# Kernel tuning notes

Measured on AMD Instinct MI355X. Metric: run time of the kernel, lower is better.

The kernel has to match this reference:

```python
import jax, jax.numpy as jnp
from jax import lax
import numpy as np

LAG, IN, H, B, T = 168, 64, 1024, 512, 168

def setup_inputs() -> dict:
    key = jax.random.key(0)
    ks = jax.random.split(key, 10)
    s1 = 1.0 / np.sqrt(LAG)
    sg = 1.0 / np.sqrt(H)
    return {
        "lag": jax.random.normal(ks[0], (B, LAG), jnp.float32),
        "curr": jax.random.normal(ks[1], (T, B, IN), jnp.float32),
        "W1": jax.random.uniform(ks[2], (H, LAG), jnp.float32, -s1, s1),
        "b1": jax.random.uniform(ks[3], (H,), jnp.float32, -s1, s1),
        "W_ih": jax.random.uniform(ks[4], (3 * H, IN), jnp.float32, -sg, sg),
        "b_ih": jax.random.uniform(ks[5], (3 * H,), jnp.float32, -sg, sg),
        "W_hh": jax.random.uniform(ks[6], (3 * H, H), jnp.float32, -sg, sg),
        "b_hh": jax.random.uniform(ks[7], (3 * H,), jnp.float32, -sg, sg),
        "W3": jax.random.uniform(ks[8], (1, H), jnp.float32, -sg, sg),
        "b3": jax.random.uniform(ks[9], (1,), jnp.float32, -sg, sg),
    }

def reference(lag, curr, W1, b1, W_ih, b_ih, W_hh, b_hh, W3, b3):
    # h_t = dense1(lag)
    h0 = lag @ W1.T + b1  # [B, H]

    def step(h, x):
        # PyTorch GRUCell math
        gi = x @ W_ih.T + b_ih   # [B, 3H]
        gh = h @ W_hh.T + b_hh   # [B, 3H]
        i_r, i_z, i_n = jnp.split(gi, 3, axis=-1)
        h_r, h_z, h_n = jnp.split(gh, 3, axis=-1)
        r = jax.nn.sigmoid(i_r + h_r)
        z = jax.nn.sigmoid(i_z + h_z)
        n = jnp.tanh(i_n + r * h_n)
        h_new = (1.0 - z) * n + z * h
        y = h_new @ W3.T + b3    # [B, 1] -> dense3 prediction
        return h_new, y[:, 0]

    _, ys = lax.scan(step, h0, curr)  # ys: [T, B]
    # torch.stack(outputs, 1).squeeze(2) -> [B, T]
    return ys.T
```

## Files before the change

kernel.cpp:

```cpp
#include <hip/hip_runtime.h>

#define T_STEPS 168
#define B_SZ 512
#define H_SZ 1024
#define IN_SZ 64
#define LAG_SZ 168
#define NWG 256
#define TPB 256

typedef __attribute__((ext_vector_type(8))) short short8;
typedef __attribute__((ext_vector_type(8))) __bf16 bf16x8;
typedef __attribute__((ext_vector_type(4))) float floatx4;

union V8u { short8 s; bf16x8 v; unsigned u[4]; };

__device__ __forceinline__ float bf2f(unsigned short u) {
    union { unsigned u; float f; } v; v.u = ((unsigned)u) << 16; return v.f;
}
__device__ __forceinline__ unsigned short f2bf(float x) {
    union { float f; unsigned u; } v; v.f = x;
    unsigned r = ((v.u >> 16) & 1u) + 0x7fffu;
    return (unsigned short)((v.u + r) >> 16);
}
__device__ __forceinline__ unsigned cvtpk(float a, float b) {
    unsigned r; asm("v_cvt_pk_bf16_f32 %0, %1, %2" : "=v"(r) : "v"(a), "v"(b)); return r;
}
__device__ __forceinline__ float lo_f(unsigned u) {
    union { unsigned x; float f; } v; v.x = u << 16; return v.f;
}
__device__ __forceinline__ float hi_f(unsigned u) {
    union { unsigned x; float f; } v; v.x = u & 0xffff0000u; return v.f;
}

#define MFB(a, b, c) __builtin_amdgcn_mfma_f32_16x16x32_bf16((a), (b), (c), 0, 0, 0)


__global__ void crnn_init2(const float* __restrict__ Whh,
                           unsigned short* __restrict__ whi,
                           unsigned short* __restrict__ h_hi,
                           unsigned int* __restrict__ flg, unsigned int* __restrict__ pop)
{
    int tid = blockIdx.x * blockDim.x + threadIdx.x;
    int nthr = gridDim.x * blockDim.x;
    for (int c = tid; c < 64 * 96 * 64; c += nthr) {
        int lane = c & 63;
        int f = (c >> 6) % 96;
        int n16 = c / (96 * 64);
        int kk = f / 3, g = f % 3;
        int l15 = lane & 15, g4 = lane >> 4;
        int row = g * H_SZ + n16 * 16 + l15;
        int col = kk * 32 + g4 * 8;
        const float* src = Whh + (size_t)row * H_SZ + col;
        short8 sh;
        #pragma unroll
        for (int e = 0; e < 8; e++) sh[e] = (short)f2bf(src[e]);
        *(short8*)(whi + (size_t)c * 8) = sh;
    }
    for (int k = tid; k < 2 * B_SZ * H_SZ; k += nthr) h_hi[k] = 0;
    for (int k = tid; k < 169 * 256; k += nthr) flg[k] = 0u;
    for (int k = tid; k < 16; k += nthr) pop[k] = 0u;
}

#define ISSUE_A(ARR, KB) { \
    unsigned va_ = voffA_cur + (unsigned)((KB) * 512); \
    asm volatile("global_load_dwordx4 %0, %1, %2 sc0"            : "=v"(ARR[0].s) : "v"(va_), "s"(sAh)); \
    asm volatile("global_load_dwordx4 %0, %1, %2 offset:64 sc0"  : "=v"(ARR[1].s) : "v"(va_), "s"(sAh)); \
    asm volatile("global_load_dwordx4 %0, %1, %2 offset:128 sc0" : "=v"(ARR[2].s) : "v"(va_), "s"(sAh)); \
    asm volatile("global_load_dwordx4 %0, %1, %2 offset:192 sc0" : "=v"(ARR[3].s) : "v"(va_), "s"(sAh)); \
    asm volatile("global_load_dwordx4 %0, %1, %2 offset:256 sc0" : "=v"(ARR[4].s) : "v"(va_), "s"(sAh)); \
    asm volatile("global_load_dwordx4 %0, %1, %2 offset:320 sc0" : "=v"(ARR[5].s) : "v"(va_), "s"(sAh)); \
    asm volatile("global_load_dwordx4 %0, %1, %2 offset:384 sc0" : "=v"(ARR[6].s) : "v"(va_), "s"(sAh)); \
    asm volatile("global_load_dwordx4 %0, %1, %2 offset:448 sc0" : "=v"(ARR[7].s) : "v"(va_), "s"(sAh)); \
}

#define KEEP8(ARR) { \
    _Pragma("unroll") \
    for (int _q = 0; _q < 8; _q++) asm volatile("" : "+v"(ARR[_q].s)); \
}

#define COMPUTE_G(ARR, KB) { \
    _Pragma("unroll") \
    for (int q = 0; q < 8; q++) { \
        const int kk = (KB) * 8 + q; \
        unsigned o_ = (unsigned)(kk * 64); \
        bf16x8 xA0 = *(const bf16x8*)((const char*)whhA + ((bb0 + o_) ^ swz)); \
        bf16x8 xA1 = *(const bf16x8*)((const char*)whhA + ((bb1 + o_) ^ swz)); \
        bf16x8 xA2 = *(const bf16x8*)((const char*)whhA + ((bb2 + o_) ^ swz)); \
        const char* pB = wfB + (size_t)kk * 3072; \
        bf16x8 h1_0 = *(const bf16x8*)(pB); \
        bf16x8 h1_1 = *(const bf16x8*)(pB + 1024); \
        bf16x8 h1_2 = *(const bf16x8*)(pB + 2048); \
        acc[0] = MFB(ARR[q].v, xA0, acc[0]); \
        acc[2] = MFB(ARR[q].v, xA1, acc[2]); \
        acc[4] = MFB(ARR[q].v, xA2, acc[4]); \
        acc[1] = MFB(ARR[q].v, h1_0, acc[1]); \
        acc[3] = MFB(ARR[q].v, h1_1, acc[3]); \
        acc[5] = MFB(ARR[q].v, h1_2, acc[5]); \
    } \
}

__launch_bounds__(TPB, 1)
__global__ void crnn_main2(
    const float* __restrict__ lag, const float* __restrict__ curr,
    const float* __restrict__ W1, const float* __restrict__ b1,
    const float* __restrict__ Wih, const float* __restrict__ b_ih,
    const float* __restrict__ Whh, const float* __restrict__ b_hh,
    const float* __restrict__ W3, const float* __restrict__ b3,
    const unsigned short* __restrict__ whi,
    unsigned short* __restrict__ h_hi,
    unsigned int* __restrict__ flg, unsigned int* __restrict__ pop,
    float* __restrict__ out)
{
    __shared__ __align__(16) unsigned short whhA[48 * 1024];
    __shared__ __align__(16) unsigned short wihh[96 * 64];
    __shared__ __align__(16) unsigned short wihl[96 * 64];
    __shared__ float red[4];
    __shared__ int sh_xr[2];

    const int tid = threadIdx.x;
    if (tid == 0) {
        unsigned x;
        asm volatile("s_getreg_b32 %0, hwreg(HW_REG_XCC_ID)" : "=s"(x));
        x &= 7u;
        unsigned rk = __hip_atomic_fetch_add(&pop[x], 1u, __ATOMIC_RELAXED, __HIP_MEMORY_SCOPE_AGENT);
        sh_xr[0] = (int)x;
        sh_xr[1] = (int)(rk & 31u);
    }
    __syncthreads();
    const int xcc = sh_xr[0];
    const int r = sh_xr[1];
    const int RB = xcc * 64;
    const int J = r * 32;
    const int n16B = 2 * r + 1;

    const int lane = tid & 63;
    const int wv = tid >> 6;
    const int l15 = lane & 15;
    const int g4 = lane >> 4;

    for (int c = tid; c < 48 * 128; c += TPB) {
        int rr = c >> 7, cc = c & 127;
        int gr = (rr >> 4) * H_SZ + J + (rr & 15);
        const float* src = Whh + (size_t)gr * H_SZ + cc * 8;
        short8 s;
        #pragma unroll
        for (int e = 0; e < 8; e++) s[e] = (short)f2bf(src[e]);
        unsigned byte = ((unsigned)(rr * 2048 + cc * 16)) ^ ((unsigned)((rr & 7) << 4));
        *(short8*)((char*)whhA + byte) = s;
    }
    for (int c = tid; c < 96 * 8; c += TPB) {
        int rr = c >> 3, cc = c & 7;
        int gr = (rr >> 5) * H_SZ + J + (rr & 31);
        const float* src = Wih + (size_t)gr * IN_SZ + cc * 8;
        short8 sh, sl;
        #pragma unroll
        for (int e = 0; e < 8; e++) {
            float v = src[e];
            unsigned short hi = f2bf(v);
            sh[e] = (short)hi;
            sl[e] = (short)f2bf(v - bf2f(hi));
        }
        unsigned byte = ((unsigned)(rr * 128 + cc * 16)) ^ ((unsigned)((rr & 7) << 4));
        *(short8*)((char*)wihh + byte) = sh;
        *(short8*)((char*)wihl + byte) = sl;
    }

    float hp[2][4];
    {
        const int brow = RB + wv * 16 + g4 * 4;
        #pragma unroll
        for (int j16 = 0; j16 < 2; j16++) {
            const int j = J + j16 * 16 + l15;
            float a[4];
            float bias = b1[j];
            #pragma unroll
            for (int e = 0; e < 4; e++) a[e] = bias;
            const float* w1p = W1 + (size_t)j * LAG_SZ;
            for (int k = 0; k < LAG_SZ; k += 4) {
                floatx4 w4 = *(const floatx4*)(w1p + k);
                #pragma unroll
                for (int e = 0; e < 4; e++) {
                    floatx4 l4 = *(const floatx4*)(lag + (size_t)(brow + e) * LAG_SZ + k);
                    a[e] += l4.x * w4.x + l4.y * w4.y + l4.z * w4.z + l4.w * w4.w;
                }
            }
            #pragma unroll
            for (int e = 0; e < 4; e++) {
                hp[j16][e] = a[e];
                h_hi[(size_t)(brow + e) * H_SZ + j] = f2bf(a[e]);
            }
        }
    }

    float br_[2], bz_[2], bni_[2], bnh_[2];
    #pragma unroll
    for (int j16 = 0; j16 < 2; j16++) {
        int j = J + j16 * 16 + l15;
        br_[j16] = b_ih[j] + b_hh[j];
        bz_[j16] = b_ih[H_SZ + j] + b_hh[H_SZ + j];
        bni_[j16] = b_ih[2 * H_SZ + j];
        bnh_[j16] = b_hh[2 * H_SZ + j];
    }

    const int ycol = (tid & 127) * 8;
    const int yrow = RB + 2 * r + (tid >> 7);
    const floatx4 yw0 = *(const floatx4*)(W3 + ycol);
    const floatx4 yw1 = *(const floatx4*)(W3 + ycol + 4);
    const float b3v = b3[0];

    const unsigned short* sAh = h_hi;
    const char* wfB = (const char*)whi + (size_t)n16B * 98304 + lane * 16;
    const unsigned voffA0 = (unsigned)(((RB + wv * 16 + l15) * H_SZ + g4 * 8) * 2);

    const unsigned bb0 = (unsigned)((0 * 16 + l15) * 2048 + g4 * 16);
    const unsigned bb1 = (unsigned)((1 * 16 + l15) * 2048 + g4 * 16);
    const unsigned bb2 = (unsigned)((2 * 16 + l15) * 2048 + g4 * 16);
    const unsigned swz = (unsigned)((l15 & 7) << 4);

    bool dead = false;
    auto set_flag = [&](int t1) {
        asm volatile("s_waitcnt vmcnt(0)" ::: "memory");
        __syncthreads();
        if (tid == 0)
            __hip_atomic_store(flg + (size_t)t1 * 256 + (size_t)xcc * 32 + (size_t)r, 1u,
                               __ATOMIC_RELAXED, __HIP_MEMORY_SCOPE_AGENT);
    };
    auto check = [&](int t, int kb) {
        if (dead) { __builtin_amdgcn_sched_barrier(0); return; }
        const unsigned int* fp = flg + (size_t)t * 256 + (size_t)xcc * 32
                               + (size_t)kb * 8 + (size_t)(lane & 7);
        int spins = 0;
        while (true) {
            unsigned v = __hip_atomic_load(fp, __ATOMIC_RELAXED, __HIP_MEMORY_SCOPE_AGENT);
            if (__ballot(v != 0) == ~0ull) break;
            __builtin_amdgcn_s_sleep(1);
            if (++spins > 2000000) { dead = true; break; }
        }
        __builtin_amdgcn_sched_barrier(0);
    };

    floatx4 acc_gi[6];
    auto compute_gi = [&](int t) {
        const float* xp = curr + (size_t)t * (B_SZ * IN_SZ)
                        + (size_t)(RB + wv * 16 + l15) * IN_SZ + g4 * 8;
        #pragma unroll
        for (int ni = 0; ni < 6; ni++) acc_gi[ni] = floatx4{0.f, 0.f, 0.f, 0.f};
        #pragma unroll
        for (int kg = 0; kg < 2; kg++) {
            floatx4 v0 = *(const floatx4*)(xp + kg * 32);
            floatx4 v1 = *(const floatx4*)(xp + kg * 32 + 4);
            V8u ah, al;
            ah.u[0] = cvtpk(v0.x, v0.y); ah.u[1] = cvtpk(v0.z, v0.w);
            ah.u[2] = cvtpk(v1.x, v1.y); ah.u[3] = cvtpk(v1.z, v1.w);
            al.u[0] = cvtpk(v0.x - lo_f(ah.u[0]), v0.y - hi_f(ah.u[0]));
            al.u[1] = cvtpk(v0.z - lo_f(ah.u[1]), v0.w - hi_f(ah.u[1]));
            al.u[2] = cvtpk(v1.x - lo_f(ah.u[2]), v1.y - hi_f(ah.u[2]));
            al.u[3] = cvtpk(v1.z - lo_f(ah.u[3]), v1.w - hi_f(ah.u[3]));
            #pragma unroll
            for (int g = 0; g < 3; g++) {
                #pragma unroll
                for (int j16 = 0; j16 < 2; j16++) {
                    int rr = g * 32 + j16 * 16 + l15;
                    unsigned byte = ((unsigned)(rr * 128 + kg * 64 + g4 * 16)) ^ ((unsigned)((rr & 7) << 4));
                    bf16x8 bh = *(const bf16x8*)((const char*)wihh + byte);
                    bf16x8 bl = *(const bf16x8*)((const char*)wihl + byte);
                    int ni = g * 2 + j16;
                    acc_gi[ni] = MFB(ah.v, bh, acc_gi[ni]);
                    acc_gi[ni] = MFB(al.v, bh, acc_gi[ni]);
                    acc_gi[ni] = MFB(ah.v, bl, acc_gi[ni]);
                }
            }
        }
    };

    auto y_reduce = [&](const V8u& yv, int tcol) {
        float p = 0.f;
        #pragma unroll
        for (int e = 0; e < 8; e++) {
            float w = (e < 4) ? yw0[e] : yw1[e - 4];
            p += bf2f((unsigned short)yv.s[e]) * w;
        }
        #pragma unroll
        for (int s = 32; s >= 1; s >>= 1) p += __shfl_down(p, s, 64);
        if (lane == 0) red[wv] = p;
        __syncthreads();
        if (tid == 0) {
            out[(size_t)(RB + 2 * r + 0) * T_STEPS + tcol] = red[0] + red[1] + b3v;
            out[(size_t)(RB + 2 * r + 1) * T_STEPS + tcol] = red[2] + red[3] + b3v;
        }
        __syncthreads();
    };

    set_flag(0);
    compute_gi(0);

    const int kb0 = r >> 3;
    int cur = 0;
    for (int t = 0; t < T_STEPS; t++) {
        const unsigned voffA_cur = voffA0 + (unsigned)cur * 1048576u;

        floatx4 acc[6];
        #pragma unroll
        for (int ni = 0; ni < 6; ni++) acc[ni] = floatx4{0.f, 0.f, 0.f, 0.f};

        V8u A0[8], A1[8], yv;
        const int k0 = kb0, k1 = (kb0 + 1) & 3, k2 = (kb0 + 2) & 3, k3 = (kb0 + 3) & 3;

        check(t, k0); ISSUE_A(A0, k0);
        check(t, k1); ISSUE_A(A1, k1);
        KEEP8(A0);  COMPUTE_G(A0, k0);
        check(t, k2); ISSUE_A(A0, k2);
        KEEP8(A1);  COMPUTE_G(A1, k1);
        check(t, k3); ISSUE_A(A1, k3);
        {
            const char* ph = (const char*)(h_hi + (size_t)cur * 524288 + (size_t)yrow * H_SZ + ycol);
            asm volatile("global_load_dwordx4 %0, %1, off sc0" : "=v"(yv.s) : "v"(ph));
        }
        KEEP8(A0);  COMPUTE_G(A0, k2);
        asm volatile("s_waitcnt vmcnt(0)" ::: "memory");
        __builtin_amdgcn_sched_barrier(0);
        KEEP8(A1);  COMPUTE_G(A1, k3);

        {
            unsigned short* nh = h_hi + (size_t)(cur ^ 1) * 524288;
            const int brow = RB + wv * 16 + g4 * 4;
            #pragma unroll
            for (int j16 = 0; j16 < 2; j16++) {
                const int j = J + j16 * 16 + l15;
                #pragma unroll
                for (int e = 0; e < 4; e++) {
                    float grv = acc[0 + j16][e] + acc_gi[0 + j16][e] + br_[j16];
                    float gzv = acc[2 + j16][e] + acc_gi[2 + j16][e] + bz_[j16];
                    float ghn = acc[4 + j16][e] + bnh_[j16];
                    float gin = acc_gi[4 + j16][e] + bni_[j16];
                    float rg = 1.f / (1.f + __expf(-grv));
                    float zg = 1.f / (1.f + __expf(-gzv));
                    float nx = gin + rg * ghn;
                    float e2 = __expf(-2.f * fabsf(nx));
                    float th = copysignf((1.f - e2) / (1.f + e2), nx);
                    float hnew = (1.f - zg) * th + zg * hp[j16][e];
                    hp[j16][e] = hnew;
                    nh[(size_t)(brow + e) * H_SZ + j] = f2bf(hnew);
                }
            }
        }

        set_flag(t + 1);
        if (t > 0) y_reduce(yv, t - 1);
        if (t + 1 < T_STEPS) compute_gi(t + 1);

        cur ^= 1;
    }

    check(T_STEPS, 0); check(T_STEPS, 1); check(T_STEPS, 2); check(T_STEPS, 3);
    {
        V8u yv;
        const char* ph = (const char*)(h_hi + (size_t)cur * 524288 + (size_t)yrow * H_SZ + ycol);
        asm volatile("global_load_dwordx4 %0, %1, off sc0" : "=v"(yv.s) : "v"(ph));
        asm volatile("s_waitcnt vmcnt(0)" ::: "memory");
        __builtin_amdgcn_sched_barrier(0);
        y_reduce(yv, T_STEPS - 1);
    }
}


extern "C" void kernel_launch(void* const* d_in, const int* in_sizes, int n_in,
                              void* d_out, int out_size, void* d_ws, size_t ws_size,
                              hipStream_t stream) {
    const float* lag  = (const float*)d_in[0];
    const float* curr = (const float*)d_in[1];
    const float* W1   = (const float*)d_in[2];
    const float* b1   = (const float*)d_in[3];
    const float* Wih  = (const float*)d_in[4];
    const float* bih  = (const float*)d_in[5];
    const float* Whh  = (const float*)d_in[6];
    const float* bhh  = (const float*)d_in[7];
    const float* W3   = (const float*)d_in[8];
    const float* b3   = (const float*)d_in[9];
    float* out = (float*)d_out;
    char* w = (char*)d_ws;

    if (ws_size < (size_t)8561728) return;

    unsigned short* whi  = (unsigned short*)(w + 0);
    unsigned short* h_hi = (unsigned short*)(w + 6291456);
    unsigned int*   flg  = (unsigned int*)(w + 8388608);
    unsigned int*   pop  = (unsigned int*)(w + 8561664);

    hipLaunchKernelGGL(crnn_init2, dim3(2048), dim3(256), 0, stream,
                       Whh, whi, h_hi, flg, pop);

    void* args[] = { (void*)&lag, (void*)&curr, (void*)&W1, (void*)&b1,
                     (void*)&Wih, (void*)&bih, (void*)&Whh, (void*)&bhh,
                     (void*)&W3, (void*)&b3, (void*)&whi,
                     (void*)&h_hi, (void*)&flg, (void*)&pop, (void*)&out };
    hipError_t e = hipLaunchCooperativeKernel((void*)crnn_main2, dim3(NWG), dim3(TPB), args, 0, stream);
    if (e != hipSuccess) {
        (void)hipGetLastError();
        hipLaunchKernelGGL(crnn_main2, dim3(NWG), dim3(TPB), 0, stream,
                           lag, curr, W1, b1, Wih, bih, Whh, bhh, W3, b3,
                           whi, h_hi, flg, pop, out);
    }
}
```

Baseline: 2.441 ms.

## Split K across two wave groups per block with LDS reduction and per-wave flags

Doubles threads per block to 512 and splits the recurrent and input-gate K dimension between two groups of four waves. The upper group stores its partial accumulators to LDS for the lower group to reduce. Readiness flags become per-wave instead of per-block, so the block-wide barrier before each flag store goes away and consumers wait on finer-grained flags. The y-output reduction is folded into the per-step barrier. This halves per-wave serial MFMA work on the latency-bound recurrent path, at the cost of an extra LDS round trip and more register and LDS pressure per block.

After: 3.379 ms. 38.4% more time.

```diff
diff --git a/kernel.cpp b/kernel.cpp
--- a/kernel.cpp
+++ b/kernel.cpp
@@ -6,7 +6,7 @@
 #define IN_SZ 64
 #define LAG_SZ 168
 #define NWG 256
-#define TPB 256
+#define TPB 512
 
 typedef __attribute__((ext_vector_type(8))) short short8;
 typedef __attribute__((ext_vector_type(8))) __bf16 bf16x8;
@@ -57,7 +57,7 @@
         *(short8*)(whi + (size_t)c * 8) = sh;
     }
     for (int k = tid; k < 2 * B_SZ * H_SZ; k += nthr) h_hi[k] = 0;
-    for (int k = tid; k < 169 * 256; k += nthr) flg[k] = 0u;
+    for (int k = tid; k < 169 * 1024; k += nthr) flg[k] = 0u;
     for (int k = tid; k < 16; k += nthr) pop[k] = 0u;
 }
 
@@ -114,7 +114,8 @@
     __shared__ __align__(16) unsigned short whhA[48 * 1024];
     __shared__ __align__(16) unsigned short wihh[96 * 64];
     __shared__ __align__(16) unsigned short wihl[96 * 64];
-    __shared__ float red[4];
+    __shared__ __align__(16) float redacc[256 * 32];
+    __shared__ float yred[2][4];
     __shared__ int sh_xr[2];
 
     const int tid = threadIdx.x;
@@ -135,6 +136,10 @@
 
     const int lane = tid & 63;
     const int wv = tid >> 6;
+    const int wvm = wv & 3;
+    const int kgK = wv >> 2;
+    const bool loW = (wv < 4);
+    const bool doY = (wvm < 2);
     const int l15 = lane & 15;
     const int g4 = lane >> 4;
 
@@ -164,10 +169,32 @@
         *(short8*)((char*)wihh + byte) = sh;
         *(short8*)((char*)wihl + byte) = sl;
     }
+    __syncthreads();
+
+    bool dead = false;
+    auto set_flag_wave = [&](int t1) {
+        asm volatile("s_waitcnt vmcnt(0)" ::: "memory");
+        if (lane == 0)
+            __hip_atomic_store(flg + (size_t)t1 * 1024 + (size_t)xcc * 128 + (size_t)r * 4 + wvm,
+                               1u, __ATOMIC_RELAXED, __HIP_MEMORY_SCOPE_AGENT);
+    };
+    auto check = [&](int t, int kb) {
+        if (dead) { __builtin_amdgcn_sched_barrier(0); return; }
+        const unsigned int* fp = flg + (size_t)t * 1024 + (size_t)xcc * 128
+                               + (size_t)kb * 32 + (size_t)(lane & 31);
+        int spins = 0;
+        while (true) {
+            unsigned v = __hip_atomic_load(fp, __ATOMIC_RELAXED, __HIP_MEMORY_SCOPE_AGENT);
+            if (__ballot(v != 0) == ~0ull) break;
+            __builtin_amdgcn_s_sleep(1);
+            if (++spins > 2000000) { dead = true; break; }
+        }
+        __builtin_amdgcn_sched_barrier(0);
+    };
 
     float hp[2][4];
-    {
-        const int brow = RB + wv * 16 + g4 * 4;
+    if (loW) {
+        const int brow = RB + wvm * 16 + g4 * 4;
         #pragma unroll
         for (int j16 = 0; j16 < 2; j16++) {
             const int j = J + j16 * 16 + l15;
@@ -190,6 +217,7 @@
                 h_hi[(size_t)(brow + e) * H_SZ + j] = f2bf(a[e]);
             }
         }
+        set_flag_wave(0);
     }
 
     float br_[2], bz_[2], bni_[2], bnh_[2];
@@ -202,99 +230,58 @@
         bnh_[j16] = b_hh[2 * H_SZ + j];
     }
 
-    const int ycol = (tid & 127) * 8;
-    const int yrow = RB + 2 * r + (tid >> 7);
+    const int ycol = kgK * 512 + lane * 8;
+    const int yrow = RB + 2 * r + (wv & 1);
+    const int yslot = kgK * 2 + (wv & 1);
     const floatx4 yw0 = *(const floatx4*)(W3 + ycol);
     const floatx4 yw1 = *(const floatx4*)(W3 + ycol + 4);
     const float b3v = b3[0];
 
     const unsigned short* sAh = h_hi;
     const char* wfB = (const char*)whi + (size_t)n16B * 98304 + lane * 16;
-    const unsigned voffA0 = (unsigned)(((RB + wv * 16 + l15) * H_SZ + g4 * 8) * 2);
+    const unsigned voffA0 = (unsigned)(((RB + wvm * 16 + l15) * H_SZ + g4 * 8) * 2);
 
     const unsigned bb0 = (unsigned)((0 * 16 + l15) * 2048 + g4 * 16);
     const unsigned bb1 = (unsigned)((1 * 16 + l15) * 2048 + g4 * 16);
     const unsigned bb2 = (unsigned)((2 * 16 + l15) * 2048 + g4 * 16);
     const unsigned swz = (unsigned)((l15 & 7) << 4);
 
-    bool dead = false;
-    auto set_flag = [&](int t1) {
-        asm volatile("s_waitcnt vmcnt(0)" ::: "memory");
-        __syncthreads();
-        if (tid == 0)
-            __hip_atomic_store(flg + (size_t)t1 * 256 + (size_t)xcc * 32 + (size_t)r, 1u,
-                               __ATOMIC_RELAXED, __HIP_MEMORY_SCOPE_AGENT);
-    };
-    auto check = [&](int t, int kb) {
-        if (dead) { __builtin_amdgcn_sched_barrier(0); return; }
-        const unsigned int* fp = flg + (size_t)t * 256 + (size_t)xcc * 32
-                               + (size_t)kb * 8 + (size_t)(lane & 7);
-        int spins = 0;
-        while (true) {
-            unsigned v = __hip_atomic_load(fp, __ATOMIC_RELAXED, __HIP_MEMORY_SCOPE_AGENT);
-            if (__ballot(v != 0) == ~0ull) break;
-            __builtin_amdgcn_s_sleep(1);
-            if (++spins > 2000000) { dead = true; break; }
-        }
-        __builtin_amdgcn_sched_barrier(0);
-    };
+    const int s_ = (r >> 3) & 1;
+    const int kb_a = kgK * 2 + s_, kb_b = kgK * 2 + (s_ ^ 1);
 
     floatx4 acc_gi[6];
     auto compute_gi = [&](int t) {
         const float* xp = curr + (size_t)t * (B_SZ * IN_SZ)
-                        + (size_t)(RB + wv * 16 + l15) * IN_SZ + g4 * 8;
+                        + (size_t)(RB + wvm * 16 + l15) * IN_SZ + g4 * 8 + kgK * 32;
         #pragma unroll
         for (int ni = 0; ni < 6; ni++) acc_gi[ni] = floatx4{0.f, 0.f, 0.f, 0.f};
-        #pragma unroll
-        for (int kg = 0; kg < 2; kg++) {
-            floatx4 v0 = *(const floatx4*)(xp + kg * 32);
-            floatx4 v1 = *(const floatx4*)(xp + kg * 32 + 4);
-            V8u ah, al;
-            ah.u[0] = cvtpk(v0.x, v0.y); ah.u[1] = cvtpk(v0.z, v0.w);
-            ah.u[2] = cvtpk(v1.x, v1.y); ah.u[3] = cvtpk(v1.z, v1.w);
-            al.u[0] = cvtpk(v0.x - lo_f(ah.u[0]), v0.y - hi_f(ah.u[0]));
-            al.u[1] = cvtpk(v0.z - lo_f(ah.u[1]), v0.w - hi_f(ah.u[1]));
-            al.u[2] = cvtpk(v1.x - lo_f(ah.u[2]), v1.y - hi_f(ah.u[2]));
-            al.u[3] = cvtpk(v1.z - lo_f(ah.u[3]), v1.w - hi_f(ah.u[3]));
-            #pragma unroll
-            for (int g = 0; g < 3; g++) {
-                #pragma unroll
-                for (int j16 = 0; j16 < 2; j16++) {
-                    int rr = g * 32 + j16 * 16 + l15;
-                    unsigned byte = ((unsigned)(rr * 128 + kg * 64 + g4 * 16)) ^ ((unsigned)((rr & 7) << 4));
-                    bf16x8 bh = *(const bf16x8*)((const char*)wihh + byte);
-                    bf16x8 bl = *(const bf16x8*)((const char*)wihl + byte);
-                    int ni = g * 2 + j16;
-                    acc_gi[ni] = MFB(ah.v, bh, acc_gi[ni]);
-                    acc_gi[ni] = MFB(al.v, bh, acc_gi[ni]);
-                    acc_gi[ni] = MFB(ah.v, bl, acc_gi[ni]);
-                }
+        floatx4 v0 = *(const floatx4*)(xp);
+        floatx4 v1 = *(const floatx4*)(xp + 4);
+        V8u ah, al;
+        ah.u[0] = cvtpk(v0.x, v0.y); ah.u[1] = cvtpk(v0.z, v0.w);
+        ah.u[2] = cvtpk(v1.x, v1.y); ah.u[3] = cvtpk(v1.z, v1.w);
+        al.u[0] = cvtpk(v0.x - lo_f(ah.u[0]), v0.y - hi_f(ah.u[0]));
+        al.u[1] = cvtpk(v0.z - lo_f(ah.u[1]), v0.w - hi_f(ah.u[1]));
+        al.u[2] = cvtpk(v1.x - lo_f(ah.u[2]), v1.y - hi_f(ah.u[2]));
+        al.u[3] = cvtpk(v1.z - lo_f(ah.u[3]), v1.w - hi_f(ah.u[3]));
+        #pragma unroll
+        for (int g = 0; g < 3; g++) {
+            #pragma unroll
+            for (int j16 = 0; j16 < 2; j16++) {
+                int rr = g * 32 + j16 * 16 + l15;
+                unsigned byte = ((unsigned)(rr * 128 + kgK * 64 + g4 * 16)) ^ ((unsigned)((rr & 7) << 4));
+                bf16x8 bh = *(const bf16x8*)((const char*)wihh + byte);
+                bf16x8 bl = *(const bf16x8*)((const char*)wihl + byte);
+                int ni = g * 2 + j16;
+                acc_gi[ni] = MFB(ah.v, bh, acc_gi[ni]);
+                acc_gi[ni] = MFB(al.v, bh, acc_gi[ni]);
+                acc_gi[ni] = MFB(ah.v, bl, acc_gi[ni]);
             }
         }
     };
 
-    auto y_reduce = [&](const V8u& yv, int tcol) {
-        float p = 0.f;
-        #pragma unroll
-        for (int e = 0; e < 8; e++) {
-            float w = (e < 4) ? yw0[e] : yw1[e - 4];
-            p += bf2f((unsigned short)yv.s[e]) * w;
-        }
-        #pragma unroll
-        for (int s = 32; s >= 1; s >>= 1) p += __shfl_down(p, s, 64);
-        if (lane == 0) red[wv] = p;
-        __syncthreads();
-        if (tid == 0) {
-            out[(size_t)(RB + 2 * r + 0) * T_STEPS + tcol] = red[0] + red[1] + b3v;
-            out[(size_t)(RB + 2 * r + 1) * T_STEPS + tcol] = red[2] + red[3] + b3v;
-        }
-        __syncthreads();
-    };
-
-    set_flag(0);
     compute_gi(0);
 
-    const int kb0 = r >> 3;
     int cur = 0;
     for (int t = 0; t < T_STEPS; t++) {
         const unsigned voffA_cur = voffA0 + (unsigned)cur * 1048576u;
@@ -304,35 +291,61 @@
         for (int ni = 0; ni < 6; ni++) acc[ni] = floatx4{0.f, 0.f, 0.f, 0.f};
 
         V8u A0[8], A1[8], yv;
-        const int k0 = kb0, k1 = (kb0 + 1) & 3, k2 = (kb0 + 2) & 3, k3 = (kb0 + 3) & 3;
-
-        check(t, k0); ISSUE_A(A0, k0);
-        check(t, k1); ISSUE_A(A1, k1);
-        KEEP8(A0);  COMPUTE_G(A0, k0);
-        check(t, k2); ISSUE_A(A0, k2);
-        KEEP8(A1);  COMPUTE_G(A1, k1);
-        check(t, k3); ISSUE_A(A1, k3);
-        {
+        check(t, kb_a); ISSUE_A(A0, kb_a);
+        check(t, kb_b); ISSUE_A(A1, kb_b);
+        if (doY) {
             const char* ph = (const char*)(h_hi + (size_t)cur * 524288 + (size_t)yrow * H_SZ + ycol);
             asm volatile("global_load_dwordx4 %0, %1, off sc0" : "=v"(yv.s) : "v"(ph));
         }
-        KEEP8(A0);  COMPUTE_G(A0, k2);
+        KEEP8(A0); COMPUTE_G(A0, kb_a);
         asm volatile("s_waitcnt vmcnt(0)" ::: "memory");
         __builtin_amdgcn_sched_barrier(0);
-        KEEP8(A1);  COMPUTE_G(A1, k3);
-
-        {
+        KEEP8(A1); COMPUTE_G(A1, kb_b);
+
+        if (doY) {
+            float p = 0.f;
+            #pragma unroll
+            for (int e = 0; e < 8; e++) {
+                float w = (e < 4) ? yw0[e] : yw1[e - 4];
+                p += bf2f((unsigned short)yv.s[e]) * w;
+            }
+            #pragma unroll
+            for (int sh = 32; sh >= 1; sh >>= 1) p += __shfl_down(p, sh, 64);
+            if (lane == 0) yred[t & 1][yslot] = p;
+        }
+
+        if (!loW) {
+            float* rb = redacc + (size_t)(tid - 256) * 32;
+            #pragma unroll
+            for (int i = 0; i < 4; i++) *(floatx4*)(rb + i * 4) = acc[i] + acc_gi[i];
+            *(floatx4*)(rb + 16) = acc[4];
+            *(floatx4*)(rb + 20) = acc[5];
+            *(floatx4*)(rb + 24) = acc_gi[4];
+            *(floatx4*)(rb + 28) = acc_gi[5];
+        }
+        __syncthreads();
+
+        if (loW) {
+            const float* rb = redacc + (size_t)tid * 32;
+            floatx4 m03[4], mhh[2], mih[2];
+            #pragma unroll
+            for (int i = 0; i < 4; i++) m03[i] = acc[i] + acc_gi[i] + *(const floatx4*)(rb + i * 4);
+            #pragma unroll
+            for (int j16 = 0; j16 < 2; j16++) {
+                mhh[j16] = acc[4 + j16] + *(const floatx4*)(rb + 16 + j16 * 4);
+                mih[j16] = acc_gi[4 + j16] + *(const floatx4*)(rb + 24 + j16 * 4);
+            }
             unsigned short* nh = h_hi + (size_t)(cur ^ 1) * 524288;
-            const int brow = RB + wv * 16 + g4 * 4;
+            const int brow = RB + wvm * 16 + g4 * 4;
             #pragma unroll
             for (int j16 = 0; j16 < 2; j16++) {
                 const int j = J + j16 * 16 + l15;
                 #pragma unroll
                 for (int e = 0; e < 4; e++) {
-                    float grv = acc[0 + j16][e] + acc_gi[0 + j16][e] + br_[j16];
-                    float gzv = acc[2 + j16][e] + acc_gi[2 + j16][e] + bz_[j16];
-                    float ghn = acc[4 + j16][e] + bnh_[j16];
-                    float gin = acc_gi[4 + j16][e] + bni_[j16];
+                    float grv = m03[0 + j16][e] + br_[j16];
+                    float gzv = m03[2 + j16][e] + bz_[j16];
+                    float ghn = mhh[j16][e] + bnh_[j16];
+                    float gin = mih[j16][e] + bni_[j16];
                     float rg = 1.f / (1.f + __expf(-grv));
                     float zg = 1.f / (1.f + __expf(-gzv));
                     float nx = gin + rg * ghn;
@@ -343,24 +356,37 @@
                     nh[(size_t)(brow + e) * H_SZ + j] = f2bf(hnew);
                 }
             }
-        }
-
-        set_flag(t + 1);
-        if (t > 0) y_reduce(yv, t - 1);
+            set_flag_wave(t + 1);
+        }
+
         if (t + 1 < T_STEPS) compute_gi(t + 1);
 
+        if (wv < 2 && lane == 0 && t > 0)
+            out[(size_t)yrow * T_STEPS + (t - 1)] = yred[t & 1][wv] + yred[t & 1][2 + wv] + b3v;
+
         cur ^= 1;
     }
 
-    check(T_STEPS, 0); check(T_STEPS, 1); check(T_STEPS, 2); check(T_STEPS, 3);
-    {
+    if (doY) {
+        check(T_STEPS, kb_a); check(T_STEPS, kb_b);
         V8u yv;
         const char* ph = (const char*)(h_hi + (size_t)cur * 524288 + (size_t)yrow * H_SZ + ycol);
         asm volatile("global_load_dwordx4 %0, %1, off sc0" : "=v"(yv.s) : "v"(ph));
         asm volatile("s_waitcnt vmcnt(0)" ::: "memory");
         __builtin_amdgcn_sched_barrier(0);
-        y_reduce(yv, T_STEPS - 1);
-    }
+        float p = 0.f;
+        #pragma unroll
+        for (int e = 0; e < 8; e++) {
+            float w = (e < 4) ? yw0[e] : yw1[e - 4];
+            p += bf2f((unsigned short)yv.s[e]) * w;
+        }
+        #pragma unroll
+        for (int sh = 32; sh >= 1; sh >>= 1) p += __shfl_down(p, sh, 64);
+        if (lane == 0) yred[0][yslot] = p;
+    }
+    __syncthreads();
+    if (wv < 2 && lane == 0)
+        out[(size_t)yrow * T_STEPS + (T_STEPS - 1)] = yred[0][wv] + yred[0][2 + wv] + b3v;
 }
 
 
@@ -380,12 +406,12 @@
     float* out = (float*)d_out;
     char* w = (char*)d_ws;
 
-    if (ws_size < (size_t)8561728) return;
+    if (ws_size < (size_t)9080896) return;
 
     unsigned short* whi  = (unsigned short*)(w + 0);
     unsigned short* h_hi = (unsigned short*)(w + 6291456);
     unsigned int*   flg  = (unsigned int*)(w + 8388608);
-    unsigned int*   pop  = (unsigned int*)(w + 8561664);
+    unsigned int*   pop  = (unsigned int*)(w + 9080832);
 
     hipLaunchKernelGGL(crnn_init2, dim3(2048), dim3(256), 0, stream,
                        Whh, whi, h_hi, flg, pop);
```

## Use per-wave flags and defer output projection via partial sums

Applied to the files above, without the earlier changes.

Replaces the per-block __syncthreads plus single flag with per-wave flags, so each wave publishes its slice of h as soon as it has written it, and consumers poll the specific producer waves they need. The per-step y reduction, which reloaded h and needed two block barriers each step, is replaced by a register-level dot product with W3 and a 16-lane shuffle reduce. These bf16 partial sums are written to a workspace buffer and summed once after the last step. This removes block barriers from the recurrent critical path. In exchange it uses more flag memory, adds an end-of-run reduction, and rounds the per-slice y partial sums to bf16, which may cost accuracy.

Measured after the change: 2.686 ms. 1.1x slower.

```diff
diff --git a/kernel.cpp b/kernel.cpp
--- a/kernel.cpp
+++ b/kernel.cpp
@@ -38,6 +38,7 @@
 __global__ void crnn_init2(const float* __restrict__ Whh,
                            unsigned short* __restrict__ whi,
                            unsigned short* __restrict__ h_hi,
+                           unsigned short* __restrict__ ypart,
                            unsigned int* __restrict__ flg, unsigned int* __restrict__ pop)
 {
     int tid = blockIdx.x * blockDim.x + threadIdx.x;
@@ -57,7 +58,8 @@
         *(short8*)(whi + (size_t)c * 8) = sh;
     }
     for (int k = tid; k < 2 * B_SZ * H_SZ; k += nthr) h_hi[k] = 0;
-    for (int k = tid; k < 169 * 256; k += nthr) flg[k] = 0u;
+    for (int k = tid; k < 168 * 8 * 64 * 32; k += nthr) ypart[k] = 0;
+    for (int k = tid; k < 169 * 1024; k += nthr) flg[k] = 0u;
     for (int k = tid; k < 16; k += nthr) pop[k] = 0u;
 }
 
@@ -107,14 +109,13 @@
     const float* __restrict__ Whh, const float* __restrict__ b_hh,
     const float* __restrict__ W3, const float* __restrict__ b3,
     const unsigned short* __restrict__ whi,
-    unsigned short* __restrict__ h_hi,
+    unsigned short* __restrict__ h_hi, unsigned short* __restrict__ ypart,
     unsigned int* __restrict__ flg, unsigned int* __restrict__ pop,
     float* __restrict__ out)
 {
     __shared__ __align__(16) unsigned short whhA[48 * 1024];
     __shared__ __align__(16) unsigned short wihh[96 * 64];
     __shared__ __align__(16) unsigned short wihl[96 * 64];
-    __shared__ float red[4];
     __shared__ int sh_xr[2];
 
     const int tid = threadIdx.x;
@@ -164,6 +165,28 @@
         *(short8*)((char*)wihh + byte) = sh;
         *(short8*)((char*)wihl + byte) = sl;
     }
+    __syncthreads();
+
+    bool dead = false;
+    auto set_flag_wave = [&](int t1) {
+        asm volatile("s_waitcnt vmcnt(0)" ::: "memory");
+        if (lane == 0)
+            __hip_atomic_store(flg + (size_t)t1 * 1024 + (size_t)xcc * 128 + (size_t)r * 4 + wv,
+                               1u, __ATOMIC_RELAXED, __HIP_MEMORY_SCOPE_AGENT);
+    };
+    auto check = [&](int t, int kb) {
+        if (dead) { __builtin_amdgcn_sched_barrier(0); return; }
+        const unsigned int* fp = flg + (size_t)t * 1024 + (size_t)xcc * 128
+                               + (size_t)(kb * 8 + (lane & 7)) * 4 + wv;
+        int spins = 0;
+        while (true) {
+            unsigned v = __hip_atomic_load(fp, __ATOMIC_RELAXED, __HIP_MEMORY_SCOPE_AGENT);
+            if (__ballot(v != 0) == ~0ull) break;
+            __builtin_amdgcn_s_sleep(1);
+            if (++spins > 2000000) { dead = true; break; }
+        }
+        __builtin_amdgcn_sched_barrier(0);
+    };
 
     float hp[2][4];
     {
@@ -191,6 +214,7 @@
             }
         }
     }
+    set_flag_wave(0);
 
     float br_[2], bz_[2], bni_[2], bnh_[2];
     #pragma unroll
@@ -201,11 +225,8 @@
         bni_[j16] = b_ih[2 * H_SZ + j];
         bnh_[j16] = b_hh[2 * H_SZ + j];
     }
-
-    const int ycol = (tid & 127) * 8;
-    const int yrow = RB + 2 * r + (tid >> 7);
-    const floatx4 yw0 = *(const floatx4*)(W3 + ycol);
-    const floatx4 yw1 = *(const floatx4*)(W3 + ycol + 4);
+    const float w3a = W3[J + l15];
+    const float w3b = W3[J + 16 + l15];
     const float b3v = b3[0];
 
     const unsigned short* sAh = h_hi;
@@ -216,28 +237,6 @@
     const unsigned bb1 = (unsigned)((1 * 16 + l15) * 2048 + g4 * 16);
     const unsigned bb2 = (unsigned)((2 * 16 + l15) * 2048 + g4 * 16);
     const unsigned swz = (unsigned)((l15 & 7) << 4);
-
-    bool dead = false;
-    auto set_flag = [&](int t1) {
-        asm volatile("s_waitcnt vmcnt(0)" ::: "memory");
-        __syncthreads();
-        if (tid == 0)
-            __hip_atomic_store(flg + (size_t)t1 * 256 + (size_t)xcc * 32 + (size_t)r, 1u,
-                               __ATOMIC_RELAXED, __HIP_MEMORY_SCOPE_AGENT);
-    };
-    auto check = [&](int t, int kb) {
-        if (dead) { __builtin_amdgcn_sched_barrier(0); return; }
-        const unsigned int* fp = flg + (size_t)t * 256 + (size_t)xcc * 32
-                               + (size_t)kb * 8 + (size_t)(lane & 7);
-        int spins = 0;
-        while (true) {
-            unsigned v = __hip_atomic_load(fp, __ATOMIC_RELAXED, __HIP_MEMORY_SCOPE_AGENT);
-            if (__ballot(v != 0) == ~0ull) break;
-            __builtin_amdgcn_s_sleep(1);
-            if (++spins > 2000000) { dead = true; break; }
-        }
-        __builtin_amdgcn_sched_barrier(0);
-    };
 
     floatx4 acc_gi[6];
     auto compute_gi = [&](int t) {
@@ -273,25 +272,6 @@
         }
     };
 
-    auto y_reduce = [&](const V8u& yv, int tcol) {
-        float p = 0.f;
-        #pragma unroll
-        for (int e = 0; e < 8; e++) {
-            float w = (e < 4) ? yw0[e] : yw1[e - 4];
-            p += bf2f((unsigned short)yv.s[e]) * w;
-        }
-        #pragma unroll
-        for (int s = 32; s >= 1; s >>= 1) p += __shfl_down(p, s, 64);
-        if (lane == 0) red[wv] = p;
-        __syncthreads();
-        if (tid == 0) {
-            out[(size_t)(RB + 2 * r + 0) * T_STEPS + tcol] = red[0] + red[1] + b3v;
-            out[(size_t)(RB + 2 * r + 1) * T_STEPS + tcol] = red[2] + red[3] + b3v;
-        }
-        __syncthreads();
-    };
-
-    set_flag(0);
     compute_gi(0);
 
     const int kb0 = r >> 3;
@@ -303,7 +283,7 @@
         #pragma unroll
         for (int ni = 0; ni < 6; ni++) acc[ni] = floatx4{0.f, 0.f, 0.f, 0.f};
 
-        V8u A0[8], A1[8], yv;
+        V8u A0[8], A1[8];
         const int k0 = kb0, k1 = (kb0 + 1) & 3, k2 = (kb0 + 2) & 3, k3 = (kb0 + 3) & 3;
 
         check(t, k0); ISSUE_A(A0, k0);
@@ -312,10 +292,6 @@
         check(t, k2); ISSUE_A(A0, k2);
         KEEP8(A1);  COMPUTE_G(A1, k1);
         check(t, k3); ISSUE_A(A1, k3);
-        {
-            const char* ph = (const char*)(h_hi + (size_t)cur * 524288 + (size_t)yrow * H_SZ + ycol);
-            asm volatile("global_load_dwordx4 %0, %1, off sc0" : "=v"(yv.s) : "v"(ph));
-        }
         KEEP8(A0);  COMPUTE_G(A0, k2);
         asm volatile("s_waitcnt vmcnt(0)" ::: "memory");
         __builtin_amdgcn_sched_barrier(0);
@@ -345,21 +321,62 @@
             }
         }
 
-        set_flag(t + 1);
-        if (t > 0) y_reduce(yv, t - 1);
+        if (t + 1 < T_STEPS) set_flag_wave(t + 1);
+
+        {
+            #pragma unroll
+            for (int e = 0; e < 4; e++) {
+                float p = w3a * hp[0][e] + w3b * hp[1][e];
+                p += __shfl_xor(p, 1, 64);
+                p += __shfl_xor(p, 2, 64);
+                p += __shfl_xor(p, 4, 64);
+                p += __shfl_xor(p, 8, 64);
+                if (l15 == 0) {
+                    int row = wv * 16 + g4 * 4 + e;
+                    ypart[((size_t)(t * 8 + xcc) * 64 + row) * 32 + r] = f2bf(p);
+                }
+            }
+        }
+
         if (t + 1 < T_STEPS) compute_gi(t + 1);
-
         cur ^= 1;
     }
 
-    check(T_STEPS, 0); check(T_STEPS, 1); check(T_STEPS, 2); check(T_STEPS, 3);
+    set_flag_wave(T_STEPS);
     {
-        V8u yv;
-        const char* ph = (const char*)(h_hi + (size_t)cur * 524288 + (size_t)yrow * H_SZ + ycol);
-        asm volatile("global_load_dwordx4 %0, %1, off sc0" : "=v"(yv.s) : "v"(ph));
+        if (!dead) {
+            const unsigned int* f1 = flg + (size_t)T_STEPS * 1024 + (size_t)xcc * 128 + lane;
+            const unsigned int* f2 = f1 + 64;
+            int spins = 0;
+            while (true) {
+                unsigned v1 = __hip_atomic_load(f1, __ATOMIC_RELAXED, __HIP_MEMORY_SCOPE_AGENT);
+                unsigned v2 = __hip_atomic_load(f2, __ATOMIC_RELAXED, __HIP_MEMORY_SCOPE_AGENT);
+                if (__ballot(v1 != 0) == ~0ull && __ballot(v2 != 0) == ~0ull) break;
+                __builtin_amdgcn_s_sleep(1);
+                if (++spins > 2000000) { dead = true; break; }
+            }
+        }
+        __builtin_amdgcn_sched_barrier(0);
+    }
+
+    for (int q = tid; q < 2 * T_STEPS; q += TPB) {
+        int t = q >> 1;
+        int rowq = 2 * r + (q & 1);
+        const char* yp = (const char*)(ypart + ((size_t)(t * 8 + xcc) * 64 + rowq) * 32);
+        V8u v0, v1, v2, v3;
+        asm volatile("global_load_dwordx4 %0, %1, off sc0" : "=v"(v0.s) : "v"(yp));
+        asm volatile("global_load_dwordx4 %0, %1, off offset:16 sc0" : "=v"(v1.s) : "v"(yp));
+        asm volatile("global_load_dwordx4 %0, %1, off offset:32 sc0" : "=v"(v2.s) : "v"(yp));
+        asm volatile("global_load_dwordx4 %0, %1, off offset:48 sc0" : "=v"(v3.s) : "v"(yp));
         asm volatile("s_waitcnt vmcnt(0)" ::: "memory");
         __builtin_amdgcn_sched_barrier(0);
-        y_reduce(yv, T_STEPS - 1);
+        float s = b3v;
+        #pragma unroll
+        for (int e = 0; e < 8; e++) {
+            s += bf2f((unsigned short)v0.s[e]) + bf2f((unsigned short)v1.s[e])
+               + bf2f((unsigned short)v2.s[e]) + bf2f((unsigned short)v3.s[e]);
+        }
+        out[(size_t)(RB + rowq) * T_STEPS + t] = s;
     }
 }
 
@@ -380,25 +397,26 @@
     float* out = (float*)d_out;
     char* w = (char*)d_ws;
 
-    if (ws_size < (size_t)8561728) return;
-
-    unsigned short* whi  = (unsigned short*)(w + 0);
-    unsigned short* h_hi = (unsigned short*)(w + 6291456);
-    unsigned int*   flg  = (unsigned int*)(w + 8388608);
-    unsigned int*   pop  = (unsigned int*)(w + 8561664);
+    if (ws_size < (size_t)14585920) return;
+
+    unsigned short* whi   = (unsigned short*)(w + 0);
+    unsigned short* h_hi  = (unsigned short*)(w + 6291456);
+    unsigned short* ypart = (unsigned short*)(w + 8388608);
+    unsigned int*   flg   = (unsigned int*)(w + 13893632);
+    unsigned int*   pop   = (unsigned int*)(w + 14585856);
 
     hipLaunchKernelGGL(crnn_init2, dim3(2048), dim3(256), 0, stream,
-                       Whh, whi, h_hi, flg, pop);
+                       Whh, whi, h_hi, ypart, flg, pop);
 
     void* args[] = { (void*)&lag, (void*)&curr, (void*)&W1, (void*)&b1,
                      (void*)&Wih, (void*)&bih, (void*)&Whh, (void*)&bhh,
                      (void*)&W3, (void*)&b3, (void*)&whi,
-                     (void*)&h_hi, (void*)&flg, (void*)&pop, (void*)&out };
+                     (void*)&h_hi, (void*)&ypart, (void*)&flg, (void*)&pop, (void*)&out };
     hipError_t e = hipLaunchCooperativeKernel((void*)crnn_main2, dim3(NWG), dim3(TPB), args, 0, stream);
     if (e != hipSuccess) {
         (void)hipGetLastError();
         hipLaunchKernelGGL(crnn_main2, dim3(NWG), dim3(TPB), 0, stream,
                            lag, curr, W1, b1, Wih, bih, Whh, bhh, W3, b3,
-                           whi, h_hi, flg, pop, out);
-    }
-}
+                           whi, h_hi, ypart, flg, pop, out);
+    }
+}
```
